# Kernel tuning notes

Measured on AMD Instinct MI355X. Metric: run time of the kernel, lower is better.

Reference implementation:

```python
import jax, jax.numpy as jnp
import numpy as np

KW = 31       # avg_pool kernel
PAD = 15      # padding (count_include_pad=True => divide by KW*KW always)


def _box_avg(x):
    # F.avg_pool2d(x, 31, stride=1, padding=15) with count_include_pad=True
    s = jax.lax.reduce_window(
        x, 0.0, jax.lax.add,
        window_dimensions=(1, 1, KW, KW),
        window_strides=(1, 1, 1, 1),
        padding=((0, 0), (0, 0), (PAD, PAD), (PAD, PAD)))
    return s / (KW * KW)


def setup_inputs() -> dict:
    key = jax.random.key(0)
    k1, k2 = jax.random.split(key)
    B, C, H, W = 64, 1, 512, 512
    pred = jax.random.normal(k1, (B, C, H, W), dtype=jnp.float32)
    mask = jax.random.uniform(k2, (B, C, H, W), dtype=jnp.float32)
    return {"pred": pred, "mask": mask}


def reference(pred, mask):
    weit = 1.0 + 5.0 * jnp.abs(_box_avg(mask) - mask)
    # stable BCE-with-logits, elementwise
    bce = jnp.maximum(pred, 0.0) - pred * mask + jnp.log1p(jnp.exp(-jnp.abs(pred)))
    # NOTE: original passes reduce='none' which PyTorch's legacy handling maps to
    # reduction='mean' -> wbce is a global scalar; the weit normalization cancels.
    wbce = bce.mean()  # scalar, broadcast over [B, C]
    p = jax.nn.sigmoid(pred)
    inter = (p * mask * weit).sum(axis=(2, 3))          # [B, C]
    union = ((p + mask) * weit).sum(axis=(2, 3))        # [B, C]
    wiou = 1.0 - (inter + 1.0) / (union - inter + 1.0)  # [B, C]
    return (wbce + wiou).mean()
```

## Files before the change

### kernel.cpp

```cpp
#include <hip/hip_runtime.h>
#include <math.h>

#define BDIM 64
#define HDIM 512
#define WDIM 512
#define KW   31
#define PAD  15
#define INV_KK (1.0f / 961.0f)
#define TH   32
#define NPIX ((size_t)BDIM * HDIM * WDIM)

#define NACC 129

__global__ void zero_acc_kernel(double* acc) {
    int i = threadIdx.x;
    if (i < NACC) acc[i] = 0.0;
}

template<int CTRL, int RMASK>
__device__ __forceinline__ float dpp_add(float p) {
    int t = __builtin_amdgcn_update_dpp(0, __builtin_bit_cast(int, p),
                                        CTRL, RMASK, 0xf, true);
    return p + __builtin_bit_cast(float, t);
}

__device__ __forceinline__ float wave_iscan(float p) {
    p = dpp_add<0x111, 0xf>(p);
    p = dpp_add<0x112, 0xf>(p);
    p = dpp_add<0x114, 0xf>(p);
    p = dpp_add<0x118, 0xf>(p);
    p = dpp_add<0x142, 0xa>(p);
    p = dpp_add<0x143, 0xc>(p);
    return p;
}

__device__ __forceinline__ float wave_iscan30(float p) {
    p = dpp_add<0x111, 0xf>(p);
    p = dpp_add<0x112, 0xf>(p);
    p = dpp_add<0x114, 0xf>(p);
    p = dpp_add<0x118, 0xf>(p);
    p = dpp_add<0x142, 0xa>(p);
    return p;
}

__device__ __forceinline__ float wave_shr1(float p) {
    int t = __builtin_amdgcn_update_dpp(0, __builtin_bit_cast(int, p),
                                        0x138 , 0xf, 0xf, true);
    return __builtin_bit_cast(float, t);
}

__global__ __launch_bounds__(512, 8)
void fused_kernel(const float* __restrict__ pred,
                  const float* __restrict__ mask,
                  double* __restrict__ acc) {
    __shared__ float red[3][8];

    const int b    = blockIdx.x;
    const int y0   = blockIdx.y * TH;
    const int x    = threadIdx.x;
    const int lane = x & 63;
    const int wv   = x >> 6;
    const int s    = wv * 64;

    const float* mbase = mask + (size_t)b * HDIM * WDIM;
    const float* pbase = pred + (size_t)b * HDIM * WDIM;

    const int acol = s - 15 + lane;
    const int bcol = s + 49 + lane;
    const int acolc = (acol < 0) ? 0 : ((acol > WDIM - 1) ? WDIM - 1 : acol);
    const int bcolc = (bcol > WDIM - 1) ? WDIM - 1 : bcol;
    const float aMul = (acol >= 0 && acol < WDIM) ? 1.f : 0.f;
    const float bMul = (lane < 30 && bcol < WDIM) ? 1.f : 0.f;

    const int tstart = y0 - PAD;
    const int tend   = y0 + TH - 1 + PAD;
    const int smax   = (tstart > 0) ? tstart : 0;

    float vsA = 0.f, vsB = 0.f;
    float bce_acc = 0.f, inter_acc = 0.f, uni_acc = 0.f;

    auto ld_halo = [&](int row, float& A, float& B) {
        int rc = row;
        if (rc < 0) rc = 0;
        if (rc > HDIM - 1) rc = HDIM - 1;
        const float* rp = mbase + (size_t)rc * WDIM;
        A = rp[acolc];
        B = rp[bcolc];
        if (row < 0 || row >= HDIM) { A = 0.f; B = 0.f; }
    };
    auto ld_sub = [&](int row, float& S, float& T) {
        int rc = (row < smax) ? smax : row;
        const float* rp = mbase + (size_t)rc * WDIM;
        S = rp[acolc];
        T = rp[bcolc];
        if (row < smax) { S = 0.f; T = 0.f; }
    };
    auto ld_emit = [&](int row, float& M, float& P) {
        int rc = row - PAD;
        if (rc > HDIM - 1) rc = HDIM - 1;
        const size_t off = (size_t)rc * WDIM + x;
        M = mbase[off];
        P = pbase[off];
    };

    auto process = [&](float A, float B, float S, float T, float M, float P) {
        vsA += A - S;
        vsB += B - T;
        float pa = wave_iscan(vsA * aMul);
        float pb = wave_iscan30(vsB * bMul);
        const float atot = __builtin_bit_cast(float,
            __builtin_amdgcn_readlane(__builtin_bit_cast(int, pa), 63));
        const float v1 = __shfl(pa, (lane + 30) & 63);
        const float v2 = __shfl(pb, (lane + 30) & 63);
        const float Phi = (lane <= 33) ? v1 : (atot + v2);
        const float Plo = wave_shr1(pa);
        const float hs  = Phi - Plo;

        const float box  = hs * INV_KK;
        const float weit = 1.f + 5.f * fabsf(box - M);
        const float e1   = __expf(-fabsf(P));
        const float bce  = fmaxf(P, 0.f) - P * M + __logf(1.f + e1);
        const float rr   = __builtin_amdgcn_rcpf(1.f + e1);
        const float sp   = (P >= 0.f) ? rr : e1 * rr;
        bce_acc   += bce;
        inter_acc += sp * M * weit;
        uni_acc   += (sp + M) * weit;
    };

    const int t0 = y0 + PAD;

    float wA0, wB0, wA1, wB1;
    float xA0, xB0, xA1, xB1;
    ld_halo(tstart,     wA0, wB0);
    ld_halo(tstart + 1, wA1, wB1);
    ld_halo(tstart + 2, xA0, xB0);
    ld_halo(tstart + 3, xA1, xB1);

    float qS0, qT0, qS1, qT1, rS0, rT0, rS1, rT1;
    float qM0, qP0, qM1, qP1, rM0, rP0, rM1, rP1;
    ld_sub (t0 - 31, qS0, qT0);
    ld_sub (t0 - 30, qS1, qT1);
    ld_sub (t0 - 29, rS0, rT0);
    ld_sub (t0 - 28, rS1, rT1);
    ld_emit(t0,      qM0, qP0);
    ld_emit(t0 + 1,  qM1, qP1);
    ld_emit(t0 + 2,  rM0, rP0);
    ld_emit(t0 + 3,  rM1, rP1);

#pragma unroll
    for (int i = 0; i < 15; ++i) {
        const int t = tstart + 2 * i;
        float nA0, nB0, nA1, nB1;
        ld_halo(t + 4, nA0, nB0);
        ld_halo(t + 5, nA1, nB1);
        vsA += wA0 + wA1;
        vsB += wB0 + wB1;
        wA0 = xA0; wB0 = xB0; wA1 = xA1; wB1 = xB1;
        xA0 = nA0; xB0 = nB0; xA1 = nA1; xB1 = nB1;
    }

    float qA0 = wA0, qB0 = wB0, qA1 = wA1, qB1 = wB1;
    float rA0 = xA0, rB0 = xB0, rA1 = xA1, rB1 = xB1;

#pragma unroll
    for (int i = 0; i < 16; ++i) {
        const int t = t0 + 2 * i;
        float nA0, nB0, nA1, nB1, nS0, nT0, nS1, nT1, nM0, nP0, nM1, nP1;
        ld_halo(t + 4, nA0, nB0);
        ld_halo(t + 5, nA1, nB1);
        ld_sub (t - 27, nS0, nT0);
        ld_sub (t - 26, nS1, nT1);
        ld_emit(t + 4, nM0, nP0);
        ld_emit(t + 5, nM1, nP1);

        process(qA0, qB0, qS0, qT0, qM0, qP0);
        process(qA1, qB1, qS1, qT1, qM1, qP1);

        qA0 = rA0; qB0 = rB0; qA1 = rA1; qB1 = rB1;
        qS0 = rS0; qT0 = rT0; qS1 = rS1; qT1 = rT1;
        qM0 = rM0; qP0 = rP0; qM1 = rP1 == rP1 ? rM1 : rM1; qP1 = rP1;
        qM1 = rM1;
        rA0 = nA0; rB0 = nB0; rA1 = nA1; rB1 = nB1;
        rS0 = nS0; rT0 = nT0; rS1 = nT1 == nT1 ? nS1 : nS1; rT1 = nT1;
        rS1 = nS1;
        rM0 = nM0; rP0 = nP0; rM1 = nM1; rP1 = nP1;
    }

#pragma unroll
    for (int off = 32; off > 0; off >>= 1) {
        bce_acc   += __shfl_down(bce_acc, off);
        inter_acc += __shfl_down(inter_acc, off);
        uni_acc   += __shfl_down(uni_acc, off);
    }
    if (lane == 0) {
        red[0][wv] = bce_acc;
        red[1][wv] = inter_acc;
        red[2][wv] = uni_acc;
    }
    __syncthreads();
    if (threadIdx.x == 0) {
        float bs = 0.f, is = 0.f, us = 0.f;
#pragma unroll
        for (int w = 0; w < 8; ++w) { bs += red[0][w]; is += red[1][w]; us += red[2][w]; }
        atomicAdd(&acc[0],      (double)bs);
        atomicAdd(&acc[1 + b],  (double)is);
        atomicAdd(&acc[65 + b], (double)us);
    }
}

__global__ void finalize_kernel(const double* __restrict__ acc, float* __restrict__ out) {
    const int b = threadIdx.x;
    double inter = acc[1 + b];
    double uni   = acc[65 + b];
    double wiou  = 1.0 - (inter + 1.0) / (uni - inter + 1.0);
#pragma unroll
    for (int off = 32; off > 0; off >>= 1) wiou += __shfl_down(wiou, off);
    if (b == 0) {
        double wbce = acc[0] / (double)NPIX;
        out[0] = (float)(wbce + wiou / (double)BDIM);
    }
}

extern "C" void kernel_launch(void* const* d_in, const int* in_sizes, int n_in,
                              void* d_out, int out_size, void* d_ws, size_t ws_size,
                              hipStream_t stream) {
    const float* pred = (const float*)d_in[0];
    const float* mask = (const float*)d_in[1];
    float* out = (float*)d_out;
    double* acc = (double*)d_ws;

    zero_acc_kernel<<<1, 256, 0, stream>>>(acc);

    dim3 grid(BDIM, HDIM / TH);
    fused_kernel<<<grid, WDIM, 0, stream>>>(pred, mask, acc);

    finalize_kernel<<<1, 64, 0, stream>>>(acc, out);
}
```

Baseline: 183.9 us.

## Predicate halo loads and roll pipelined row loops to cut code size

Replaces clamped-address loads plus multiply-by-zero masking with predicated loads that skip out-of-range rows and columns, which removes the aMul/bMul multiplies from the scans. The fully unrolled warm-up and main loops become rolled loops; the main loop processes four rows per iteration with a ping-pong q/r register set instead of shifting copies. The aim is a smaller instruction footprint, less register pressure and fewer wasted loads. The cost is branch/exec-mask overhead, and rolled loops give the compiler less room to schedule loads early.

```diff
diff --git a/kernel.cpp b/kernel.cpp
--- a/kernel.cpp
+++ b/kernel.cpp
@@ -67,10 +67,8 @@
 
     const int acol = s - 15 + lane;
     const int bcol = s + 49 + lane;
-    const int acolc = (acol < 0) ? 0 : ((acol > WDIM - 1) ? WDIM - 1 : acol);
-    const int bcolc = (bcol > WDIM - 1) ? WDIM - 1 : bcol;
-    const float aMul = (acol >= 0 && acol < WDIM) ? 1.f : 0.f;
-    const float bMul = (lane < 30 && bcol < WDIM) ? 1.f : 0.f;
+    const bool a_ok = (acol >= 0) && (acol < WDIM);
+    const bool b_ok = (lane < 30) && (bcol < WDIM);
 
     const int tstart = y0 - PAD;
     const int tend   = y0 + TH - 1 + PAD;
@@ -80,34 +78,35 @@
     float bce_acc = 0.f, inter_acc = 0.f, uni_acc = 0.f;
 
     auto ld_halo = [&](int row, float& A, float& B) {
-        int rc = row;
-        if (rc < 0) rc = 0;
-        if (rc > HDIM - 1) rc = HDIM - 1;
-        const float* rp = mbase + (size_t)rc * WDIM;
-        A = rp[acolc];
-        B = rp[bcolc];
-        if (row < 0 || row >= HDIM) { A = 0.f; B = 0.f; }
+        A = 0.f; B = 0.f;
+        if (row >= 0 && row < HDIM) {
+            const float* rp = mbase + (size_t)row * WDIM;
+            if (a_ok) A = rp[acol];
+            if (b_ok) B = rp[bcol];
+        }
     };
     auto ld_sub = [&](int row, float& S, float& T) {
-        int rc = (row < smax) ? smax : row;
-        const float* rp = mbase + (size_t)rc * WDIM;
-        S = rp[acolc];
-        T = rp[bcolc];
-        if (row < smax) { S = 0.f; T = 0.f; }
+        S = 0.f; T = 0.f;
+        if (row >= smax) {
+            const float* rp = mbase + (size_t)row * WDIM;
+            if (a_ok) S = rp[acol];
+            if (b_ok) T = rp[bcol];
+        }
     };
     auto ld_emit = [&](int row, float& M, float& P) {
-        int rc = row - PAD;
-        if (rc > HDIM - 1) rc = HDIM - 1;
-        const size_t off = (size_t)rc * WDIM + x;
-        M = mbase[off];
-        P = pbase[off];
+        M = 0.f; P = 0.f;
+        if (row <= tend) {
+            const size_t off = (size_t)(row - PAD) * WDIM + x;
+            M = mbase[off];
+            P = pbase[off];
+        }
     };
 
     auto process = [&](float A, float B, float S, float T, float M, float P) {
         vsA += A - S;
         vsB += B - T;
-        float pa = wave_iscan(vsA * aMul);
-        float pb = wave_iscan30(vsB * bMul);
+        float pa = wave_iscan(vsA);
+        float pb = wave_iscan30(vsB);
         const float atot = __builtin_bit_cast(float,
             __builtin_amdgcn_readlane(__builtin_bit_cast(int, pa), 63));
         const float v1 = __shfl(pa, (lane + 30) & 63);
@@ -147,7 +146,7 @@
     ld_emit(t0 + 2,  rM0, rP0);
     ld_emit(t0 + 3,  rM1, rP1);
 
-#pragma unroll
+#pragma unroll 1
     for (int i = 0; i < 15; ++i) {
         const int t = tstart + 2 * i;
         float nA0, nB0, nA1, nB1;
@@ -158,32 +157,28 @@
         wA0 = xA0; wB0 = xB0; wA1 = xA1; wB1 = xB1;
         xA0 = nA0; xB0 = nB0; xA1 = nA1; xB1 = nB1;
     }
-
     float qA0 = wA0, qB0 = wB0, qA1 = wA1, qB1 = wB1;
     float rA0 = xA0, rB0 = xB0, rA1 = xA1, rB1 = xB1;
 
-#pragma unroll
-    for (int i = 0; i < 16; ++i) {
-        const int t = t0 + 2 * i;
-        float nA0, nB0, nA1, nB1, nS0, nT0, nS1, nT1, nM0, nP0, nM1, nP1;
-        ld_halo(t + 4, nA0, nB0);
-        ld_halo(t + 5, nA1, nB1);
-        ld_sub (t - 27, nS0, nT0);
-        ld_sub (t - 26, nS1, nT1);
-        ld_emit(t + 4, nM0, nP0);
-        ld_emit(t + 5, nM1, nP1);
-
+#pragma unroll 1
+    for (int k = 0; k < 8; ++k) {
+        const int t = t0 + 4 * k;
         process(qA0, qB0, qS0, qT0, qM0, qP0);
         process(qA1, qB1, qS1, qT1, qM1, qP1);
-
-        qA0 = rA0; qB0 = rB0; qA1 = rA1; qB1 = rB1;
-        qS0 = rS0; qT0 = rT0; qS1 = rS1; qT1 = rT1;
-        qM0 = rM0; qP0 = rP0; qM1 = rP1 == rP1 ? rM1 : rM1; qP1 = rP1;
-        qM1 = rM1;
-        rA0 = nA0; rB0 = nB0; rA1 = nA1; rB1 = nB1;
-        rS0 = nS0; rT0 = nT0; rS1 = nT1 == nT1 ? nS1 : nS1; rT1 = nT1;
-        rS1 = nS1;
-        rM0 = nM0; rP0 = nP0; rM1 = nM1; rP1 = nP1;
+        ld_halo(t + 4, qA0, qB0);
+        ld_halo(t + 5, qA1, qB1);
+        ld_sub (t - 27, qS0, qT0);
+        ld_sub (t - 26, qS1, qT1);
+        ld_emit(t + 4, qM0, qP0);
+        ld_emit(t + 5, qM1, qP1);
+        process(rA0, rB0, rS0, rT0, rM0, rP0);
+        process(rA1, rB1, rS1, rT1, rM1, rP1);
+        ld_halo(t + 6, rA0, rB0);
+        ld_halo(t + 7, rA1, rB1);
+        ld_sub (t - 25, rS0, rT0);
+        ld_sub (t - 24, rS1, rT1);
+        ld_emit(t + 6, rM0, rP0);
+        ld_emit(t + 7, rM1, rP1);
     }
 
 #pragma unroll
```

Result: faster. 170.3 us (-7.4%).
